# Kernel optimization log

Measured on AMD Instinct MI355X. Metric: run time of the kernel, lower is better.

The kernel has to match this reference:

```python
import jax, jax.numpy as jnp
import numpy as np

N_NODES = 50000
N_EDGES = 200000
D_IN = 128
D = 256
N_LAYERS = 4
N_REL = 4
NUM_M = 1024
NUM_R = 64
DIM_Y = 2
LAM_VI = 0.1
LAM_REG = 0.1
TEMP = 0.3  # RelaxedBernoulli temperature used by FNP sample_bipartite
EPS = 1e-8


def _glorot(key, shape):
    fan_in = shape[-2] if len(shape) >= 2 else shape[0]
    return (jax.random.normal(key, shape, dtype=jnp.float32) / np.float32(np.sqrt(fan_in)))


def setup_inputs() -> dict:
    key = jax.random.key(0)
    ks = jax.random.split(key, 16)
    x = jax.random.normal(ks[0], (N_NODES, D_IN), jnp.float32)
    edge_index = jax.random.randint(ks[1], (2, N_EDGES), 0, N_NODES)
    edge_type = jax.random.randint(ks[2], (N_EDGES,), 0, N_REL)
    batch = jnp.sort(jax.random.randint(ks[3], (N_NODES,), 0, NUM_M))
    yM = jax.random.randint(ks[4], (NUM_M,), 0, DIM_Y)
    yR = jax.random.randint(ks[5], (NUM_R,), 0, DIM_Y)
    H_R = jax.random.normal(ks[6], (NUM_R, D), jnp.float32)
    node_W = _glorot(ks[7], (D_IN, D)); node_b = jnp.zeros((D,), jnp.float32)
    gcn_Wr = _glorot(ks[8], (N_LAYERS, N_REL, D, D))
    gcn_Wroot = _glorot(ks[9], (N_LAYERS, D, D))
    gcn_b = jnp.zeros((N_LAYERS, D), jnp.float32)
    pg_logscale = jnp.array([0.5 * np.log(D)], jnp.float32)  # log(sqrt(dim_u)) init
    pu_W = _glorot(ks[10], (D, 2 * D)); pu_b = jnp.zeros((2 * D,), jnp.float32)
    qz_W = _glorot(ks[11], (D, 2 * D)); qz_b = jnp.zeros((2 * D,), jnp.float32)
    out_W1 = _glorot(ks[12], (2 * D, 256)); out_b1 = jnp.zeros((256,), jnp.float32)
    out_W2 = _glorot(ks[13], (256, DIM_Y)); out_b2 = jnp.zeros((DIM_Y,), jnp.float32)
    return dict(x=x, edge_index=edge_index, edge_type=edge_type, batch=batch, yM=yM, yR=yR,
                H_R=H_R, node_W=node_W, node_b=node_b, gcn_Wr=gcn_Wr, gcn_Wroot=gcn_Wroot,
                gcn_b=gcn_b, pg_logscale=pg_logscale, pu_W=pu_W, pu_b=pu_b, qz_W=qz_W,
                qz_b=qz_b, out_W1=out_W1, out_b1=out_b1, out_W2=out_W2, out_b2=out_b2)


def _cond_trans(x, edge_index, edge_type, batch, node_W, node_b, gcn_Wr, gcn_Wroot, gcn_b):
    # AtomEncoder replaced by Linear (num_relations==1 branch); then 4 RGCNConv layers
    n = x.shape[0]
    src, dst = edge_index[0], edge_index[1]
    feats = x @ node_W + node_b
    for l in range(N_LAYERS):
        # per-relation transform of all nodes: [N_REL, N, D]
        h_rel = jnp.einsum('nd,rdh->rnh', feats, gcn_Wr[l])
        msg = h_rel[edge_type, src]  # gather per-edge messages [E, D]
        comp = edge_type * n + dst   # (relation, dst) composite segment id
        cnt = jax.ops.segment_sum(jnp.ones((msg.shape[0],), feats.dtype), comp,
                                  num_segments=N_REL * n)
        msg = msg / jnp.clip(cnt[comp], 1.0)[:, None]  # mean aggregation per relation
        agg = jax.ops.segment_sum(msg, dst, num_segments=n)
        feats = agg + feats @ gcn_Wroot[l] + gcn_b[l]
        if l < N_LAYERS - 1:
            feats = jax.nn.relu(feats)
    gsum = jax.ops.segment_sum(feats, batch, num_segments=NUM_M)
    gcnt = jax.ops.segment_sum(jnp.ones((n,), feats.dtype), batch, num_segments=NUM_M)
    return gsum / jnp.clip(gcnt, 1.0)[:, None]  # global_mean_pool


def _normal_logprob(v, mean, logscale):
    return -0.5 * np.float32(np.log(2 * np.pi)) - logscale - 0.5 * ((v - mean) * jnp.exp(-logscale)) ** 2


def _logitexp(logp):
    # logit of exp(logp): logp - log(1 - exp(logp))
    return logp - jnp.log(jnp.clip(-jnp.expm1(logp), 1e-20))


def reference(x, edge_index, edge_type, batch, yM, yR, H_R, node_W, node_b, gcn_Wr,
              gcn_Wroot, gcn_b, pg_logscale, pu_W, pu_b, qz_W, qz_b, out_W1, out_b1,
              out_W2, out_b2):
    H_M = _cond_trans(x, edge_index, edge_type, batch, node_W, node_b, gcn_Wr, gcn_Wroot, gcn_b)
    H_all = jnp.concatenate([H_R, H_M], axis=0)
    key = jax.random.key(42)
    k_u, k_a, k_zm, k_zr = jax.random.split(key, 4)

    # p_u: ReLU -> Linear -> split mean / logscale; reparameterized sample
    pu = jax.nn.relu(H_all) @ pu_W + pu_b
    pu_mean, pu_ls = pu[:, :D], pu[:, D:]
    u = pu_mean + jnp.exp(pu_ls) * jax.random.normal(k_u, pu_mean.shape, pu_mean.dtype)
    u_R, u_M = u[:NUM_R], u[NUM_R:]

    # sample_bipartite(u_M, u_R, pairwise_g): relaxed Bernoulli over pairwise logits
    d2 = jnp.sum((u_M[:, None, :] - u_R[None, :, :]) ** 2, axis=-1)  # [M, R]
    logits_A = _logitexp(-0.5 * d2 / jnp.exp(pg_logscale[0]))
    U = jax.random.uniform(k_a, logits_A.shape, minval=1e-6, maxval=1.0 - 1e-6)
    A = jax.nn.sigmoid((logits_A + jnp.log(U) - jnp.log1p(-U)) / TEMP)
    An = A / (jnp.sum(A, axis=1, keepdims=True) + EPS)  # norm_graph

    # q_z head
    qz = jax.nn.relu(H_all) @ qz_W + qz_b
    qz_mean, qz_ls = qz[:, :D], qz[:, D:]
    z_M = qz_mean[NUM_R:] + jnp.exp(qz_ls[NUM_R:]) * jax.random.normal(k_zm, (NUM_M, D), qz_mean.dtype)
    pz_mean_M = An @ qz_mean[:NUM_R]
    pz_ls_M = An @ qz_ls[:NUM_R]
    log_pqz_M = jnp.sum(_normal_logprob(z_M, pz_mean_M, pz_ls_M)
                        - _normal_logprob(z_M, qz_mean[NUM_R:], qz_ls[NUM_R:]))
    z_R = qz_mean[:NUM_R] + jnp.exp(qz_ls[:NUM_R]) * jax.random.normal(k_zr, (NUM_R, D), qz_mean.dtype)

    # prediction head (use_plus=True -> concat z and u)
    rep_M = jnp.concatenate([z_M, u_M], axis=1)
    logits_M = jax.nn.relu(rep_M @ out_W1 + out_b1) @ out_W2 + out_b2
    log_pyM = jnp.take_along_axis(jax.nn.log_softmax(logits_M, axis=-1), yM[:, None], axis=1)[:, 0]
    prediction_loss = -(jnp.sum(log_pyM) + LAM_VI * log_pqz_M) / np.float32(NUM_M)

    rep_R = jnp.concatenate([z_R, u_R], axis=1)
    logits_R = jax.nn.relu(rep_R @ out_W1 + out_b1) @ out_W2 + out_b2
    rationale_loss = -jnp.mean(jnp.take_along_axis(jax.nn.log_softmax(logits_R, axis=-1), yR[:, None], axis=1)[:, 0])

    # mode 'E' distance regularizer
    pd = jnp.sqrt(jnp.clip(jnp.sum((u_R[:, None, :] - u_M[None, :, :]) ** 2, axis=-1), 1e-12))  # [R, M]
    idx = jnp.arange(NUM_R // 2)[:, None] + (1 - yM)[None, :] * (NUM_R // 2)
    reg = jnp.mean(jnp.take_along_axis(pd, idx, axis=0))

    return prediction_loss + rationale_loss - LAM_REG * reg
```

## Files before the change

### kernel.cpp

```cpp
#include <hip/hip_runtime.h>
#include <stdint.h>

#define N_NODESC 50000
#define N_EDGESC 200000
#define D_INC 128
#define DC 256
#define N_LAYERSC 4
#define N_RELC 4
#define NUM_MC 1024
#define NUM_RC 64
#define NBLK_SCAN ((N_NODESC + 255) / 256)

typedef __attribute__((ext_vector_type(4))) float floatx4;
typedef __attribute__((ext_vector_type(8))) short short8;

__host__ __device__ __forceinline__ uint32_t rotl32(uint32_t x, int r){ return (x<<r)|(x>>(32-r)); }

__host__ __device__ inline void tf2x32(uint32_t k0, uint32_t k1, uint32_t x0, uint32_t x1,
                                       uint32_t* o0, uint32_t* o1){
  uint32_t k2 = k0 ^ k1 ^ 0x1BD11BDAu;
#define TFR(r) { x0 += x1; x1 = rotl32(x1, (r)); x1 ^= x0; }
  x0 += k0; x1 += k1;
  TFR(13) TFR(15) TFR(26) TFR(6)
  x0 += k1; x1 += k2 + 1u;
  TFR(17) TFR(29) TFR(16) TFR(24)
  x0 += k2; x1 += k0 + 2u;
  TFR(13) TFR(15) TFR(26) TFR(6)
  x0 += k0; x1 += k1 + 3u;
  TFR(17) TFR(29) TFR(16) TFR(24)
  x0 += k1; x1 += k2 + 4u;
  TFR(13) TFR(15) TFR(26) TFR(6)
  x0 += k2; x1 += k0 + 5u;
#undef TFR
  *o0 = x0; *o1 = x1;
}

__device__ __forceinline__ float erfinv_f32(float x){
  float w = -log1pf(-x*x);
  float p;
  if (w < 5.0f){
    w -= 2.5f;
    p = 2.81022636e-08f;
    p = fmaf(p, w, 3.43273939e-07f);
    p = fmaf(p, w, -3.5233877e-06f);
    p = fmaf(p, w, -4.39150654e-06f);
    p = fmaf(p, w, 0.00021858087f);
    p = fmaf(p, w, -0.00125372503f);
    p = fmaf(p, w, -0.00417768164f);
    p = fmaf(p, w, 0.246640727f);
    p = fmaf(p, w, 1.50140941f);
  } else {
    w = sqrtf(w) - 3.0f;
    p = -0.000200214257f;
    p = fmaf(p, w, 0.000100950558f);
    p = fmaf(p, w, 0.00134934322f);
    p = fmaf(p, w, -0.00367342844f);
    p = fmaf(p, w, 0.00573950773f);
    p = fmaf(p, w, -0.0076224613f);
    p = fmaf(p, w, 0.00943887047f);
    p = fmaf(p, w, 1.00167406f);
    p = fmaf(p, w, 2.83297682f);
  }
  return p*x;
}

__device__ __forceinline__ float bits_to_unit(uint32_t b){
  return __uint_as_float((b >> 9) | 0x3f800000u) - 1.0f;
}

__device__ __forceinline__ float bits_to_normal(uint32_t b){
  float f = bits_to_unit(b);
  const float lo = -0.99999994f;
  float u = f * (1.0f - lo) + lo;
  u = fmaxf(u, lo);
  return 1.41421356f * erfinv_f32(u);
}

__device__ __forceinline__ float waveReduce(float v){
  #pragma unroll
  for (int m = 1; m < 64; m <<= 1) v += __shfl_xor(v, m, 64);
  return v;
}

__device__ __forceinline__ ushort f2bf(float f){
  uint32_t u = __float_as_uint(f);
  uint32_t r = u + 0x7fffu + ((u>>16)&1u);
  return (ushort)(r>>16);
}
__device__ __forceinline__ float bf2f(ushort h){
  return __uint_as_float(((uint32_t)h)<<16);
}

typedef const __attribute__((address_space(1))) void* gas_t;
typedef __attribute__((address_space(3))) void* las_t;
__device__ __forceinline__ void gld16(const void* g, void* l){
  __builtin_amdgcn_global_load_lds((gas_t)g, (las_t)l, 16, 0, 0);
}

__global__ __launch_bounds__(256) void k_zero4(float4* p, int n4){
  int i = blockIdx.x*256 + threadIdx.x;
  if (i < n4) p[i] = make_float4(0.f,0.f,0.f,0.f);
}

__global__ __launch_bounds__(256) void k_count(const int* __restrict__ ei, const int* __restrict__ et,
                                               float* __restrict__ cnt, int* __restrict__ deg){
  int e = blockIdx.x*256 + threadIdx.x;
  if (e >= N_EDGESC) return;
  int r = et[e], dstv = ei[N_EDGESC + e];
  atomicAdd(&cnt[(size_t)r*N_NODESC + dstv], 1.0f);
  atomicAdd(&deg[dstv], 1);
}

__global__ __launch_bounds__(256) void k_scan1(const int* __restrict__ deg, int* __restrict__ bsum){
  int i = blockIdx.x*256 + threadIdx.x;
  int v = (i < N_NODESC) ? deg[i] : 0;
  #pragma unroll
  for (int m = 1; m < 64; m <<= 1) v += __shfl_xor(v, m, 64);
  __shared__ int ws_[4];
  if ((threadIdx.x & 63) == 0) ws_[threadIdx.x >> 6] = v;
  __syncthreads();
  if (threadIdx.x == 0) bsum[blockIdx.x] = ws_[0]+ws_[1]+ws_[2]+ws_[3];
}

__global__ __launch_bounds__(256) void k_scan2(int* __restrict__ bsum, int* __restrict__ boff){
  __shared__ int s[256];
  int t = threadIdx.x;
  s[t] = (t < NBLK_SCAN) ? bsum[t] : 0;
  __syncthreads();
  if (t == 0){
    int run = 0;
    for (int i = 0; i < NBLK_SCAN; i++){ int v = s[i]; s[i] = run; run += v; }
  }
  __syncthreads();
  if (t < NBLK_SCAN) boff[t] = s[t];
}

__global__ __launch_bounds__(256) void k_scan3(const int* __restrict__ deg, const int* __restrict__ boff,
                                               int* __restrict__ rowptr){
  int i = blockIdx.x*256 + threadIdx.x;
  int lane = threadIdx.x & 63, w = threadIdx.x >> 6;
  int d = (i < N_NODESC) ? deg[i] : 0;
  int v = d;
  #pragma unroll
  for (int off = 1; off < 64; off <<= 1){
    int t = __shfl_up(v, off, 64);
    if (lane >= off) v += t;
  }
  __shared__ int wt[4];
  if (lane == 63) wt[w] = v;
  __syncthreads();
  int wo = 0;
  for (int k = 0; k < w; k++) wo += wt[k];
  int ex = boff[blockIdx.x] + wo + v - d;
  if (i <= N_NODESC) rowptr[i] = ex;
}

__global__ __launch_bounds__(256) void k_fill2(const int* __restrict__ ei, const int* __restrict__ et,
                                               const float* __restrict__ cnt, const int* __restrict__ rowptr,
                                               int* __restrict__ cursor, int* __restrict__ ep,
                                               float* __restrict__ einvc){
  int e = blockIdx.x*256 + threadIdx.x;
  if (e >= N_EDGESC) return;
  int src = ei[e], dstv = ei[N_EDGESC + e], r = et[e];
  int pos = rowptr[dstv] + atomicAdd(&cursor[dstv], 1);
  ep[pos] = src | (r << 16);
  einvc[pos] = 1.0f / fmaxf(cnt[(size_t)r*N_NODESC + dstv], 1.0f);
}

__global__ __launch_bounds__(256) void k_bnd(const int* __restrict__ batch, int* __restrict__ grow){
  int i = blockIdx.x*256 + threadIdx.x;
  if (i >= N_NODESC) return;
  int b = batch[i];
  if (i == 0){ for (int g = 0; g <= b; g++) grow[g] = 0; }
  else {
    int pb = batch[i-1];
    for (int g = pb+1; g <= b; g++) grow[g] = i;
  }
  if (i == N_NODESC-1){ for (int g = b+1; g <= NUM_MC; g++) grow[g] = N_NODESC; }
}

#define SEG0 (N_NODESC*D_INC/4)
#define SEG1 (DC*D_INC)
#define SEG2 (N_LAYERSC*DC*1280)
#define SEG3 (DC*1024)
#define SEG4 (DC*512)
#define SEG5 1024
__global__ __launch_bounds__(256) void k_prep(const float* __restrict__ x, ushort* __restrict__ xb,
                                              const float* __restrict__ node_W, ushort* __restrict__ node_Wt,
                                              const float* __restrict__ Wroot, const float* __restrict__ Wr,
                                              ushort* __restrict__ Wcat,
                                              const float* __restrict__ pu_W, const float* __restrict__ qz_W,
                                              float* __restrict__ pqW,
                                              const float* __restrict__ out_W1, ushort* __restrict__ W1t,
                                              const float* __restrict__ pu_b, const float* __restrict__ qz_b,
                                              float* __restrict__ pqb){
  int idx = blockIdx.x*256 + threadIdx.x;
  if (idx < SEG0){
    float4 v = ((const float4*)x)[idx];
    ushort4 o; o.x=f2bf(v.x); o.y=f2bf(v.y); o.z=f2bf(v.z); o.w=f2bf(v.w);
    ((ushort4*)xb)[idx] = o;
    return;
  }
  idx -= SEG0;
  if (idx < SEG1){
    int n = idx >> 7, k = idx & 127;
    node_Wt[idx] = f2bf(node_W[(size_t)k*DC + n]);
    return;
  }
  idx -= SEG1;
  if (idx < SEG2){
    int l = idx / (DC*1280), rem = idx - l*(DC*1280);
    int n = rem / 1280, k = rem - n*1280;
    float v;
    if (k < DC) v = Wroot[((size_t)l*DC + k)*DC + n];
    else {
      int kk = k - DC, r = kk >> 8, kr = kk & 255;
      v = Wr[(((size_t)l*N_RELC + r)*DC + kr)*DC + n];
    }
    Wcat[idx] = f2bf(v);
    return;
  }
  idx -= SEG2;
  if (idx < SEG3){
    int k = idx >> 10, n = idx & 1023;
    pqW[idx] = (n < 512) ? pu_W[(size_t)k*512 + n] : qz_W[(size_t)k*512 + (n-512)];
    return;
  }
  idx -= SEG3;
  if (idx < SEG4){
    int n = idx >> 9, k = idx & 511;
    W1t[idx] = f2bf(out_W1[(size_t)k*DC + n]);
    return;
  }
  idx -= SEG4;
  if (idx < SEG5){
    pqb[idx] = (idx < 512) ? pu_b[idx] : qz_b[idx-512];
  }
}

__global__ __launch_bounds__(256) void k_agg(const ushort* __restrict__ curb, ushort* __restrict__ agg,
                                             const int* __restrict__ rowptr, const int* __restrict__ ep,
                                             const float* __restrict__ einvc){
  int dstv = blockIdx.x*4 + (threadIdx.x >> 6);
  if (dstv >= N_NODESC) return;
  int lane = threadIdx.x & 63;
  int beg = rowptr[dstv], end = rowptr[dstv+1];
  float4 s0 = {0,0,0,0}, s1 = {0,0,0,0}, s2 = {0,0,0,0}, s3 = {0,0,0,0};
  int p = beg;
  while (p < end){
    int nb = end - p; if (nb > 8) nb = 8;
    int pk[8]; float ic[8]; ushort4 h[8];
    #pragma unroll
    for (int j = 0; j < 8; j++) if (j < nb){ pk[j] = ep[p+j]; ic[j] = einvc[p+j]; }
    #pragma unroll
    for (int j = 0; j < 8; j++) if (j < nb)
      h[j] = *(const ushort4*)(curb + (size_t)(pk[j] & 0xffff)*DC + lane*4);
    #pragma unroll
    for (int j = 0; j < 8; j++) if (j < nb){
      float c = ic[j];
      int r = pk[j] >> 16;
      float hx = bf2f(h[j].x)*c, hy = bf2f(h[j].y)*c, hz = bf2f(h[j].z)*c, hw = bf2f(h[j].w)*c;
      if (r == 0){ s0.x+=hx; s0.y+=hy; s0.z+=hz; s0.w+=hw; }
      else if (r == 1){ s1.x+=hx; s1.y+=hy; s1.z+=hz; s1.w+=hw; }
      else if (r == 2){ s2.x+=hx; s2.y+=hy; s2.z+=hz; s2.w+=hw; }
      else { s3.x+=hx; s3.y+=hy; s3.z+=hz; s3.w+=hw; }
    }
    p += nb;
  }
  ushort* ab = agg + (size_t)dstv*1024 + lane*4;
  ushort4 o;
  o.x=f2bf(s0.x); o.y=f2bf(s0.y); o.z=f2bf(s0.z); o.w=f2bf(s0.w); *(ushort4*)(ab       ) = o;
  o.x=f2bf(s1.x); o.y=f2bf(s1.y); o.z=f2bf(s1.z); o.w=f2bf(s1.w); *(ushort4*)(ab + 256 ) = o;
  o.x=f2bf(s2.x); o.y=f2bf(s2.y); o.z=f2bf(s2.z); o.w=f2bf(s2.w); *(ushort4*)(ab + 512 ) = o;
  o.x=f2bf(s3.x); o.y=f2bf(s3.y); o.z=f2bf(s3.z); o.w=f2bf(s3.w); *(ushort4*)(ab + 768 ) = o;
}

__global__ __launch_bounds__(256) void k_pool(const ushort* __restrict__ featsb, const int* __restrict__ grow,
                                              const float* __restrict__ H_R, float* __restrict__ Hrelu){
  int row = blockIdx.x*4 + (threadIdx.x >> 6);
  if (row >= NUM_RC + NUM_MC) return;
  int lane = threadIdx.x & 63;
  float4 v;
  if (row < NUM_RC){
    v = *(const float4*)(H_R + (size_t)row*DC + lane*4);
  } else {
    int g = row - NUM_RC;
    int beg = grow[g], end = grow[g+1];
    float ax=0.f, ay=0.f, az=0.f, aw=0.f;
    for (int i = beg; i < end; i++){
      const ushort4 f = *(const ushort4*)(featsb + (size_t)i*DC + lane*4);
      ax += bf2f(f.x); ay += bf2f(f.y); az += bf2f(f.z); aw += bf2f(f.w);
    }
    float ic = 1.0f / fmaxf((float)(end-beg), 1.0f);
    v.x = ax*ic; v.y = ay*ic; v.z = az*ic; v.w = aw*ic;
  }
  v.x = fmaxf(v.x,0.f); v.y = fmaxf(v.y,0.f); v.z = fmaxf(v.z,0.f); v.w = fmaxf(v.w,0.f);
  *(float4*)(Hrelu + (size_t)row*DC + lane*4) = v;
}

__global__ __launch_bounds__(256) void k_gemm_bf16(
    const ushort* __restrict__ A1, int lda1,
    const ushort* __restrict__ A2, int lda2, int Ksplit,
    const ushort* __restrict__ Bt, int ldb,
    void* __restrict__ Cout0, int ldc,
    int M, int N, int K,
    const float* __restrict__ bias, int flags)
{
  __shared__ ushort As[64*64];
  __shared__ ushort Bs[128*64];
  const int tid = threadIdx.x;
  const int wave = tid >> 6, lane = tid & 63;
  const int m0 = blockIdx.y * 64, n0 = blockIdx.x * 128;
  const int wn = wave * 32;
  const int qa = lane >> 4, lm = lane & 15;

  const int lrow = lane >> 3;
  const int slot = lane & 7;

  floatx4 acc[4][2] = {};

  for (int k0 = 0; k0 < K; k0 += 64){
    const ushort* a_base; int a_ld, acol;
    if (k0 < Ksplit){ a_base = A1; a_ld = lda1; acol = k0; }
    else            { a_base = A2; a_ld = lda2; acol = k0 - Ksplit; }
    #pragma unroll
    for (int t = 0; t < 2; t++){
      int rb = wave*16 + t*8;
      int rr = rb + lrow;
      int gl = slot ^ (rr & 7);
      int ar = m0 + rr; if (ar > M-1) ar = M-1;
      gld16(a_base + (size_t)ar*a_ld + acol + gl*8, As + (size_t)rb*64 + lane*8);
    }
    #pragma unroll
    for (int t = 0; t < 4; t++){
      int rb = wave*32 + t*8;
      int rr = rb + lrow;
      int gl = slot ^ (rr & 7);
      gld16(Bt + (size_t)(n0 + rr)*ldb + k0 + gl*8, Bs + (size_t)rb*64 + lane*8);
    }
    __syncthreads();
    #pragma unroll
    for (int kk2 = 0; kk2 < 2; kk2++){
      short8 af[4], bfv[2];
      #pragma unroll
      for (int mt = 0; mt < 4; mt++){
        int rr = mt*16 + lm;
        af[mt] = *(const short8*)(As + (size_t)rr*64 + (size_t)(((kk2*4 + qa) ^ (rr & 7)))*8);
      }
      #pragma unroll
      for (int nt = 0; nt < 2; nt++){
        int rr = wn + nt*16 + lm;
        bfv[nt] = *(const short8*)(Bs + (size_t)rr*64 + (size_t)(((kk2*4 + qa) ^ (rr & 7)))*8);
      }
      #pragma unroll
      for (int mt = 0; mt < 4; mt++)
        #pragma unroll
        for (int nt = 0; nt < 2; nt++)
          acc[mt][nt] = __builtin_amdgcn_mfma_f32_16x16x32_bf16(af[mt], bfv[nt], acc[mt][nt], 0, 0, 0);
    }
    __syncthreads();
  }

  #pragma unroll
  for (int mt = 0; mt < 4; mt++){
    #pragma unroll
    for (int i = 0; i < 4; i++){
      int row = m0 + mt*16 + qa*4 + i;
      if (row >= M) continue;
      #pragma unroll
      for (int nt = 0; nt < 2; nt++){
        int col = n0 + wn + nt*16 + lm;
        float v = acc[mt][nt][i];
        if (flags & 2) v += bias[col];
        if (flags & 4) v = fmaxf(v, 0.0f);
        if (flags & 1)
          ((ushort*)Cout0)[(size_t)row*ldc + col] = f2bf(v);
        else
          ((float*)Cout0)[(size_t)row*ldc + col] = v;
      }
    }
  }
}

__global__ __launch_bounds__(256) void k_gemm(
    const float* __restrict__ A, int lda,
    const float* __restrict__ B, int ldb,
    float* __restrict__ C, int ldc,
    int M, int N, int K,
    const float* __restrict__ bias, int flags)
{
  __shared__ __align__(16) float Asm[64][36];
  __shared__ __align__(16) float Bsm[32][64];
  const int tid = threadIdx.x;
  const int tx = tid & 15, ty = tid >> 4;
  const int m0 = blockIdx.y * 64, n0 = blockIdx.x * 64;
  const int am = tid >> 2, ak = (tid & 3) * 8;
  const int bk = tid >> 3, bn = (tid & 7) * 8;
  float acc[4][4] = {};
  for (int k0 = 0; k0 < K; k0 += 32){
    float4 a0, a1;
    int arow = m0 + am;
    if (arow < M){
      const float* ap = A + (size_t)arow*lda + (k0 + ak);
      a0 = *(const float4*)ap;
      a1 = *(const float4*)(ap + 4);
    } else {
      a0 = make_float4(0,0,0,0); a1 = a0;
    }
    const float* bp = B + (size_t)(k0 + bk)*ldb + (n0 + bn);
    float4 b0v = *(const float4*)bp;
    float4 b1v = *(const float4*)(bp + 4);
    *(float4*)&Asm[am][ak]   = a0;
    *(float4*)&Asm[am][ak+4] = a1;
    *(float4*)&Bsm[bk][bn]   = b0v;
    *(float4*)&Bsm[bk][bn+4] = b1v;
    __syncthreads();
    #pragma unroll
    for (int kk = 0; kk < 32; ++kk){
      float av[4], bv[4];
      #pragma unroll
      for (int i=0;i<4;i++) av[i] = Asm[ty*4+i][kk];
      #pragma unroll
      for (int j=0;j<4;j++) bv[j] = Bsm[kk][tx*4+j];
      #pragma unroll
      for (int i=0;i<4;i++)
        #pragma unroll
        for (int j=0;j<4;j++)
          acc[i][j] = fmaf(av[i], bv[j], acc[i][j]);
    }
    __syncthreads();
  }
  #pragma unroll
  for (int i=0;i<4;i++){
    int row = m0 + ty*4 + i;
    if (row >= M) continue;
    #pragma unroll
    for (int j=0;j<4;j++){
      int col = n0 + tx*4 + j;
      float v = acc[i][j];
      if (flags & 2) v += bias[col];
      if (flags & 4) v = fmaxf(v, 0.0f);
      C[(size_t)row*ldc + col] = v;
    }
  }
}

__global__ __launch_bounds__(256) void k_sample_u(const float* __restrict__ pq, float* __restrict__ u,
                                                  ushort* __restrict__ repb,
                                                  uint32_t k0, uint32_t k1){
  const int half = (1088*DC)/2;
  int j = blockIdx.x*256 + threadIdx.x;
  if (j >= half) return;
  uint32_t o0, o1;
  tf2x32(k0, k1, (uint32_t)j, (uint32_t)(j + half), &o0, &o1);
  #pragma unroll
  for (int t = 0; t < 2; t++){
    int i = j + t*half;
    uint32_t bits = t ? o1 : o0;
    int row = i >> 8, col = i & 255;
    const float* pr = pq + (size_t)row*1024;
    float val = pr[col] + expf(pr[256 + col]) * bits_to_normal(bits);
    u[i] = val;
    repb[(size_t)row*512 + 256 + col] = f2bf(val);
  }
}

__global__ __launch_bounds__(256) void k_sample_zM(const float* __restrict__ pq, float* __restrict__ zM,
                                                   ushort* __restrict__ repb,
                                                   uint32_t k0, uint32_t k1){
  const int half = (NUM_MC*DC)/2;
  int j = blockIdx.x*256 + threadIdx.x;
  if (j >= half) return;
  uint32_t o0, o1;
  tf2x32(k0, k1, (uint32_t)j, (uint32_t)(j + half), &o0, &o1);
  #pragma unroll
  for (int t = 0; t < 2; t++){
    int i = j + t*half;
    uint32_t bits = t ? o1 : o0;
    int m = i >> 8, col = i & 255;
    const float* pr = pq + (size_t)(NUM_RC + m)*1024;
    float val = pr[512 + col] + expf(pr[768 + col]) * bits_to_normal(bits);
    zM[i] = val;
    repb[(size_t)(NUM_RC + m)*512 + col] = f2bf(val);
  }
}

__global__ __launch_bounds__(256) void k_sample_zR(const float* __restrict__ pq, ushort* __restrict__ repb,
                                                   uint32_t k0, uint32_t k1){
  const int half = (NUM_RC*DC)/2;
  int j = blockIdx.x*256 + threadIdx.x;
  if (j >= half) return;
  uint32_t o0, o1;
  tf2x32(k0, k1, (uint32_t)j, (uint32_t)(j + half), &o0, &o1);
  #pragma unroll
  for (int t = 0; t < 2; t++){
    int i = j + t*half;
    uint32_t bits = t ? o1 : o0;
    int r = i >> 8, col = i & 255;
    const float* pr = pq + (size_t)r*1024;
    float val = pr[512 + col] + expf(pr[768 + col]) * bits_to_normal(bits);
    repb[(size_t)r*512 + col] = f2bf(val);
  }
}

__global__ __launch_bounds__(64) void k_d2(const float* __restrict__ u, float* __restrict__ d2){
  int m = blockIdx.x, r = threadIdx.x;
  const float4* um = (const float4*)(u + (size_t)(NUM_RC + m)*DC);
  const float4* ur = (const float4*)(u + (size_t)r*DC);
  float s = 0.f;
  #pragma unroll 4
  for (int d = 0; d < DC/4; ++d){
    float4 a = um[d], b = ur[d];
    float dx = a.x-b.x, dy = a.y-b.y, dz = a.z-b.z, dw = a.w-b.w;
    s = fmaf(dx,dx, fmaf(dy,dy, fmaf(dz,dz, fmaf(dw,dw, s))));
  }
  d2[m*NUM_RC + r] = s;
}

__device__ __forceinline__ void A_elem(float* An, const float* d2, int i, uint32_t bits, float inv_s){
  float logp = -0.5f * d2[i] * inv_s;
  float la = logp - logf(fmaxf(-expm1f(logp), 1e-20f));
  float f = bits_to_unit(bits);
  const float mn = 1e-6f, mx = 0.999999f;
  float U = fmaxf(f*(mx-mn) + mn, mn);
  float g = (la + logf(U) - log1pf(-U)) / 0.3f;
  An[i] = 1.0f / (1.0f + expf(-g));
}

__global__ __launch_bounds__(256) void k_A(const float* __restrict__ d2, const float* __restrict__ pg,
                                           float* __restrict__ An, uint32_t k0, uint32_t k1){
  const int HALF = (NUM_MC*NUM_RC)/2;
  int j = blockIdx.x*256 + threadIdx.x;
  if (j >= HALF) return;
  uint32_t o0, o1;
  tf2x32(k0, k1, (uint32_t)j, (uint32_t)(j + HALF), &o0, &o1);
  float inv_s = expf(-pg[0]);
  A_elem(An, d2, j, o0, inv_s);
  A_elem(An, d2, j + HALF, o1, inv_s);
}

__global__ __launch_bounds__(64) void k_rownorm(float* __restrict__ An){
  int m = blockIdx.x, r = threadIdx.x;
  float v = An[m*NUM_RC + r];
  float s = waveReduce(v);
  An[m*NUM_RC + r] = v / (s + 1e-8f);
}

__global__ __launch_bounds__(256) void k_logpqz(const float* __restrict__ zM, const float* __restrict__ pzcat,
                                                const float* __restrict__ pq, float* __restrict__ scal){
  int idx = blockIdx.x*256 + threadIdx.x;
  int m = idx >> 8, d = idx & 255;
  float z  = zM[idx];
  float pm = pzcat[(size_t)m*512 + d];
  float pl = pzcat[(size_t)m*512 + 256 + d];
  const float* qrow = pq + (size_t)(NUM_RC + m)*1024;
  float qm = qrow[512 + d], ql = qrow[768 + d];
  float tp = (z - pm) * expf(-pl);
  float tq = (z - qm) * expf(-ql);
  float term = (-pl - 0.5f*tp*tp) - (-ql - 0.5f*tq*tq);
  float s = waveReduce(term);
  if ((threadIdx.x & 63) == 0) atomicAdd(&scal[0], s);
}

__global__ __launch_bounds__(256) void k_out_head(const float* __restrict__ hid, const float* __restrict__ W2,
                                                  const float* __restrict__ b2, const int* __restrict__ yM,
                                                  const int* __restrict__ yR, float* __restrict__ scal){
  int wave = threadIdx.x >> 6, lane = threadIdx.x & 63;
  int row = blockIdx.x*4 + wave;
  if (row >= NUM_RC + NUM_MC) return;
  const float* h = hid + (size_t)row*256;
  float p0 = 0.f, p1 = 0.f;
  #pragma unroll
  for (int c = 0; c < 4; c++){
    int d = lane*4 + c;
    float hv = h[d];
    p0 = fmaf(hv, W2[d*2+0], p0);
    p1 = fmaf(hv, W2[d*2+1], p1);
  }
  p0 = waveReduce(p0);
  p1 = waveReduce(p1);
  if (lane == 0){
    float l0 = p0 + b2[0], l1 = p1 + b2[1];
    float mx = fmaxf(l0, l1);
    float lse = mx + logf(expf(l0-mx) + expf(l1-mx));
    int y = (row < NUM_RC) ? yR[row] : yM[row - NUM_RC];
    float lp = ((y == 0) ? l0 : l1) - lse;
    atomicAdd((row < NUM_RC) ? &scal[2] : &scal[1], lp);
  }
}

__global__ __launch_bounds__(256) void k_reg(const float* __restrict__ d2, const int* __restrict__ yM,
                                             float* __restrict__ scal){
  int t = blockIdx.x*256 + threadIdx.x;
  float v = 0.f;
  if (t < 32*1024){
    int i = t >> 10, m = t & 1023;
    int col = i + (1 - yM[m]) * 32;
    v = sqrtf(fmaxf(d2[m*NUM_RC + col], 1e-12f));
  }
  float s = waveReduce(v);
  if ((threadIdx.x & 63) == 0) atomicAdd(&scal[3], s);
}

__global__ void k_final(const float* __restrict__ scal, float* __restrict__ out){
  float pred = -(scal[1] + 0.1f*scal[0]) / 1024.0f;
  float rat  = -scal[2] / 64.0f;
  float regm = scal[3] / 32768.0f;
  out[0] = pred + rat - 0.1f*regm;
}

extern "C" void kernel_launch(void* const* d_in, const int* in_sizes, int n_in,
                              void* d_out, int out_size, void* d_ws, size_t ws_size,
                              hipStream_t stream) {
  const float* x         = (const float*)d_in[0];
  const int*   edge_index= (const int*)  d_in[1];
  const int*   edge_type = (const int*)  d_in[2];
  const int*   batch     = (const int*)  d_in[3];
  const int*   yM        = (const int*)  d_in[4];
  const int*   yR        = (const int*)  d_in[5];
  const float* H_R       = (const float*)d_in[6];
  const float* node_W    = (const float*)d_in[7];
  const float* node_b    = (const float*)d_in[8];
  const float* gcn_Wr    = (const float*)d_in[9];
  const float* gcn_Wroot = (const float*)d_in[10];
  const float* gcn_b     = (const float*)d_in[11];
  const float* pg_ls     = (const float*)d_in[12];
  const float* pu_W      = (const float*)d_in[13];
  const float* pu_b      = (const float*)d_in[14];
  const float* qz_W      = (const float*)d_in[15];
  const float* qz_b      = (const float*)d_in[16];
  const float* out_W1    = (const float*)d_in[17];
  const float* out_b1    = (const float*)d_in[18];
  const float* out_W2    = (const float*)d_in[19];
  const float* out_b2    = (const float*)d_in[20];
  float* out = (float*)d_out;

  char* base = (char*)d_ws;
  size_t off = 0;
  auto ALLOC = [&](size_t nbytes)->void*{
    void* p = base + off; off += (nbytes + 255) & ~(size_t)255; return p;
  };
  ushort* curb_a  = (ushort*)ALLOC((size_t)N_NODESC*DC*2);
  ushort* curb_b  = (ushort*)ALLOC((size_t)N_NODESC*DC*2);
  ushort* agg     = (ushort*)ALLOC((size_t)N_NODESC*1024*2);
  ushort* xb      = (ushort*)ALLOC((size_t)N_NODESC*D_INC*2);
  ushort* node_Wt = (ushort*)ALLOC((size_t)SEG1*2);
  ushort* Wcat    = (ushort*)ALLOC((size_t)SEG2*2);
  float*  pqW     = (float*) ALLOC((size_t)SEG3*4);
  ushort* W1t     = (ushort*)ALLOC((size_t)SEG4*2);
  float*  pqb     = (float*) ALLOC((size_t)SEG5*4);
  float*  zgrp    = (float*) ALLOC((size_t)(N_RELC*N_NODESC + N_NODESC + N_NODESC + 16)*4);
  float*  cnt     = zgrp;
  int*    deg     = (int*)(cnt + (size_t)N_RELC*N_NODESC);
  int*    cursor  = deg + N_NODESC;
  float*  scal    = (float*)(cursor + N_NODESC);
  int*    rowptr  = (int*)   ALLOC((size_t)(N_NODESC+1)*4);
  int*    bsum    = (int*)   ALLOC((size_t)NBLK_SCAN*4);
  int*    boff    = (int*)   ALLOC((size_t)NBLK_SCAN*4);
  int*    ep      = (int*)   ALLOC((size_t)N_EDGESC*4);
  float*  einvc   = (float*) ALLOC((size_t)N_EDGESC*4);
  int*    grow    = (int*)   ALLOC((size_t)(NUM_MC+1)*4);
  float*  Hrelu   = (float*) ALLOC((size_t)1088*DC*4);
  float*  pq      = (float*) ALLOC((size_t)1088*1024*4);
  float*  u       = (float*) ALLOC((size_t)1088*DC*4);
  ushort* repb    = (ushort*)ALLOC((size_t)1088*512*2);
  float*  zM      = (float*) ALLOC((size_t)NUM_MC*DC*4);
  float*  d2      = (float*) ALLOC((size_t)NUM_MC*NUM_RC*4);
  float*  An      = (float*) ALLOC((size_t)NUM_MC*NUM_RC*4);
  float*  pzcat   = (float*) ALLOC((size_t)NUM_MC*512*4);
  float*  hid     = (float*) ALLOC((size_t)1088*256*4);
  (void)ws_size; (void)in_sizes; (void)n_in; (void)out_size;

  uint32_t ya0,ya1,yb0,yb1,yc0,yc1,yd0,yd1;
  tf2x32(0u,42u, 0u,4u, &ya0,&ya1);
  tf2x32(0u,42u, 1u,5u, &yb0,&yb1);
  tf2x32(0u,42u, 2u,6u, &yc0,&yc1);
  tf2x32(0u,42u, 3u,7u, &yd0,&yd1);
  const uint32_t ku0=ya0,  ku1=yb0;
  const uint32_t ka0=yc0,  ka1=yd0;
  const uint32_t kzm0=ya1, kzm1=yb1;
  const uint32_t kzr0=yc1, kzr1=yd1;

  auto GEMM = [&](const float* A, int lda, const float* B, int ldb, float* C, int ldc,
                  int M, int N, int K, const float* bias, int flags){
    k_gemm<<<dim3(N/64, (M+63)/64), dim3(256), 0, stream>>>(A, lda, B, ldb, C, ldc, M, N, K, bias, flags);
  };
  auto BGEMM = [&](const ushort* A1, int lda1, const ushort* A2, int lda2, int Ksplit,
                   const ushort* Bt, int ldb, void* C, int ldc,
                   int M, int N, int K, const float* bias, int flags){
    k_gemm_bf16<<<dim3(N/128, (M+63)/64), dim3(256), 0, stream>>>(
        A1, lda1, A2, lda2, Ksplit, Bt, ldb, C, ldc, M, N, K, bias, flags);
  };

  {
    int n4 = (N_RELC*N_NODESC + 2*N_NODESC + 16)/4;
    k_zero4<<<dim3((n4+255)/256), dim3(256), 0, stream>>>((float4*)zgrp, n4);
  }
  k_count<<<dim3((N_EDGESC+255)/256), dim3(256), 0, stream>>>(edge_index, edge_type, cnt, deg);
  k_scan1<<<dim3(NBLK_SCAN), dim3(256), 0, stream>>>(deg, bsum);
  k_scan2<<<dim3(1), dim3(256), 0, stream>>>(bsum, boff);
  k_scan3<<<dim3(NBLK_SCAN), dim3(256), 0, stream>>>(deg, boff, rowptr);
  k_fill2<<<dim3((N_EDGESC+255)/256), dim3(256), 0, stream>>>(edge_index, edge_type, cnt, rowptr, cursor, ep, einvc);
  k_bnd  <<<dim3((N_NODESC+255)/256), dim3(256), 0, stream>>>(batch, grow);
  {
    int total = SEG0+SEG1+SEG2+SEG3+SEG4+SEG5;
    k_prep<<<dim3((total+255)/256), dim3(256), 0, stream>>>(
        x, xb, node_W, node_Wt, gcn_Wroot, gcn_Wr, Wcat, pu_W, qz_W, pqW, out_W1, W1t, pu_b, qz_b, pqb);
  }

  BGEMM(xb, D_INC, xb, D_INC, D_INC, node_Wt, D_INC, curb_a, DC, N_NODESC, DC, D_INC, node_b, 1|2);

  ushort* cur = curb_a; ushort* nxt = curb_b;
  for (int l = 0; l < N_LAYERSC; l++){
    k_agg<<<dim3((N_NODESC+3)/4), dim3(256), 0, stream>>>(cur, agg, rowptr, ep, einvc);
    int fl = 1 | 2 | ((l < N_LAYERSC-1) ? 4 : 0);
    BGEMM(cur, DC, agg, 1024, DC, Wcat + (size_t)l*DC*1280, 1280, nxt, DC,
          N_NODESC, DC, 1280, gcn_b + l*DC, fl);
    ushort* t = nxt; nxt = cur; cur = t;
  }

  k_pool<<<dim3((NUM_RC+NUM_MC+3)/4), dim3(256), 0, stream>>>(cur, grow, H_R, Hrelu);

  GEMM(Hrelu, DC, pqW, 1024, pq, 1024, 1088, 1024, DC, pqb, 2);

  k_sample_u<<<dim3(544), dim3(256), 0, stream>>>(pq, u, repb, ku0, ku1);

  k_d2<<<dim3(NUM_MC), dim3(64), 0, stream>>>(u, d2);
  k_A <<<dim3(128), dim3(256), 0, stream>>>(d2, pg_ls, An, ka0, ka1);
  k_rownorm<<<dim3(NUM_MC), dim3(64), 0, stream>>>(An);

  GEMM(An, NUM_RC, pq + 512, 1024, pzcat, 512, NUM_MC, 512, NUM_RC, nullptr, 0);

  k_sample_zM<<<dim3(512), dim3(256), 0, stream>>>(pq, zM, repb, kzm0, kzm1);
  k_logpqz<<<dim3(1024), dim3(256), 0, stream>>>(zM, pzcat, pq, scal);
  k_sample_zR<<<dim3(32), dim3(256), 0, stream>>>(pq, repb, kzr0, kzr1);

  BGEMM(repb, 512, repb, 512, 512, W1t, 512, hid, 256, NUM_RC+NUM_MC, 256, 512, out_b1, 2|4);
  k_out_head<<<dim3((NUM_RC+NUM_MC)/4), dim3(256), 0, stream>>>(hid, out_W2, out_b2, yM, yR, scal);

  k_reg<<<dim3(128), dim3(256), 0, stream>>>(d2, yM, scal);
  k_final<<<dim3(1), dim3(1), 0, stream>>>(scal, out);
}
```

Measured before the change: 742.0 us.

## Use half-wave-per-node aggregation, 8-wave bf16 GEMM, and batched pool loads

The aggregation kernel now gives each destination node 32 lanes that load 8 bf16 values each, so 8 nodes run per block with wider 16-byte gathers and FMA accumulation. The bf16 GEMM moves from 4 to 8 waves per block on the same 64x128 tile, which halves the per-wave accumulator footprint and the per-thread tile loads. The pooling loop batches 4 row loads at a time to expose more memory parallelism. These changes aim at the memory-bound gather and the GEMM's latency hiding, at the cost of more register-heavy aggregation lanes and more waves sharing the same LDS tile.

```diff
diff --git a/kernel.cpp b/kernel.cpp
--- a/kernel.cpp
+++ b/kernel.cpp
@@ -241,38 +241,55 @@
 __global__ __launch_bounds__(256) void k_agg(const ushort* __restrict__ curb, ushort* __restrict__ agg,
                                              const int* __restrict__ rowptr, const int* __restrict__ ep,
                                              const float* __restrict__ einvc){
-  int dstv = blockIdx.x*4 + (threadIdx.x >> 6);
+  int halfid = threadIdx.x >> 5;
+  int dstv = blockIdx.x*8 + halfid;
   if (dstv >= N_NODESC) return;
-  int lane = threadIdx.x & 63;
+  int lane = threadIdx.x & 31;
   int beg = rowptr[dstv], end = rowptr[dstv+1];
-  float4 s0 = {0,0,0,0}, s1 = {0,0,0,0}, s2 = {0,0,0,0}, s3 = {0,0,0,0};
+  float s0[8] = {}, s1[8] = {}, s2[8] = {}, s3[8] = {};
   int p = beg;
   while (p < end){
     int nb = end - p; if (nb > 8) nb = 8;
-    int pk[8]; float ic[8]; ushort4 h[8];
+    int pk[8]; float ic[8]; short8 h[8];
     #pragma unroll
     for (int j = 0; j < 8; j++) if (j < nb){ pk[j] = ep[p+j]; ic[j] = einvc[p+j]; }
     #pragma unroll
     for (int j = 0; j < 8; j++) if (j < nb)
-      h[j] = *(const ushort4*)(curb + (size_t)(pk[j] & 0xffff)*DC + lane*4);
+      h[j] = *(const short8*)(curb + (size_t)(pk[j] & 0xffff)*DC + lane*8);
     #pragma unroll
     for (int j = 0; j < 8; j++) if (j < nb){
       float c = ic[j];
       int r = pk[j] >> 16;
-      float hx = bf2f(h[j].x)*c, hy = bf2f(h[j].y)*c, hz = bf2f(h[j].z)*c, hw = bf2f(h[j].w)*c;
-      if (r == 0){ s0.x+=hx; s0.y+=hy; s0.z+=hz; s0.w+=hw; }
-      else if (r == 1){ s1.x+=hx; s1.y+=hy; s1.z+=hz; s1.w+=hw; }
-      else if (r == 2){ s2.x+=hx; s2.y+=hy; s2.z+=hz; s2.w+=hw; }
-      else { s3.x+=hx; s3.y+=hy; s3.z+=hz; s3.w+=hw; }
+      if (r == 0){
+        #pragma unroll
+        for (int e = 0; e < 8; e++) s0[e] = fmaf(bf2f((ushort)h[j][e]), c, s0[e]);
+      } else if (r == 1){
+        #pragma unroll
+        for (int e = 0; e < 8; e++) s1[e] = fmaf(bf2f((ushort)h[j][e]), c, s1[e]);
+      } else if (r == 2){
+        #pragma unroll
+        for (int e = 0; e < 8; e++) s2[e] = fmaf(bf2f((ushort)h[j][e]), c, s2[e]);
+      } else {
+        #pragma unroll
+        for (int e = 0; e < 8; e++) s3[e] = fmaf(bf2f((ushort)h[j][e]), c, s3[e]);
+      }
     }
     p += nb;
   }
-  ushort* ab = agg + (size_t)dstv*1024 + lane*4;
-  ushort4 o;
-  o.x=f2bf(s0.x); o.y=f2bf(s0.y); o.z=f2bf(s0.z); o.w=f2bf(s0.w); *(ushort4*)(ab       ) = o;
-  o.x=f2bf(s1.x); o.y=f2bf(s1.y); o.z=f2bf(s1.z); o.w=f2bf(s1.w); *(ushort4*)(ab + 256 ) = o;
-  o.x=f2bf(s2.x); o.y=f2bf(s2.y); o.z=f2bf(s2.z); o.w=f2bf(s2.w); *(ushort4*)(ab + 512 ) = o;
-  o.x=f2bf(s3.x); o.y=f2bf(s3.y); o.z=f2bf(s3.z); o.w=f2bf(s3.w); *(ushort4*)(ab + 768 ) = o;
+  ushort* ab = agg + (size_t)dstv*1024 + lane*8;
+  short8 o;
+  #pragma unroll
+  for (int e = 0; e < 8; e++) o[e] = (short)f2bf(s0[e]);
+  *(short8*)(ab      ) = o;
+  #pragma unroll
+  for (int e = 0; e < 8; e++) o[e] = (short)f2bf(s1[e]);
+  *(short8*)(ab + 256) = o;
+  #pragma unroll
+  for (int e = 0; e < 8; e++) o[e] = (short)f2bf(s2[e]);
+  *(short8*)(ab + 512) = o;
+  #pragma unroll
+  for (int e = 0; e < 8; e++) o[e] = (short)f2bf(s3[e]);
+  *(short8*)(ab + 768) = o;
 }
 
 __global__ __launch_bounds__(256) void k_pool(const ushort* __restrict__ featsb, const int* __restrict__ grow,
@@ -287,9 +304,18 @@
     int g = row - NUM_RC;
     int beg = grow[g], end = grow[g+1];
     float ax=0.f, ay=0.f, az=0.f, aw=0.f;
-    for (int i = beg; i < end; i++){
-      const ushort4 f = *(const ushort4*)(featsb + (size_t)i*DC + lane*4);
-      ax += bf2f(f.x); ay += bf2f(f.y); az += bf2f(f.z); aw += bf2f(f.w);
+    int i = beg;
+    while (i < end){
+      int nb = end - i; if (nb > 4) nb = 4;
+      ushort4 f[4];
+      #pragma unroll
+      for (int j = 0; j < 4; j++) if (j < nb)
+        f[j] = *(const ushort4*)(featsb + (size_t)(i+j)*DC + lane*4);
+      #pragma unroll
+      for (int j = 0; j < 4; j++) if (j < nb){
+        ax += bf2f(f[j].x); ay += bf2f(f[j].y); az += bf2f(f[j].z); aw += bf2f(f[j].w);
+      }
+      i += nb;
     }
     float ic = 1.0f / fmaxf((float)(end-beg), 1.0f);
     v.x = ax*ic; v.y = ay*ic; v.z = az*ic; v.w = aw*ic;
@@ -298,7 +324,7 @@
   *(float4*)(Hrelu + (size_t)row*DC + lane*4) = v;
 }
 
-__global__ __launch_bounds__(256) void k_gemm_bf16(
+__global__ __launch_bounds__(512) void k_gemm_bf16(
     const ushort* __restrict__ A1, int lda1,
     const ushort* __restrict__ A2, int lda2, int Ksplit,
     const ushort* __restrict__ Bt, int ldb,
@@ -311,40 +337,39 @@
   const int tid = threadIdx.x;
   const int wave = tid >> 6, lane = tid & 63;
   const int m0 = blockIdx.y * 64, n0 = blockIdx.x * 128;
-  const int wn = wave * 32;
+  const int wm = (wave >> 2) * 32;
+  const int wn = (wave & 3) * 32;
   const int qa = lane >> 4, lm = lane & 15;
 
   const int lrow = lane >> 3;
   const int slot = lane & 7;
 
-  floatx4 acc[4][2] = {};
+  floatx4 acc[2][2] = {};
 
   for (int k0 = 0; k0 < K; k0 += 64){
     const ushort* a_base; int a_ld, acol;
     if (k0 < Ksplit){ a_base = A1; a_ld = lda1; acol = k0; }
     else            { a_base = A2; a_ld = lda2; acol = k0 - Ksplit; }
+    {
+      int rr = wave*8 + lrow;
+      int gl = slot ^ (rr & 7);
+      int ar = m0 + rr; if (ar > M-1) ar = M-1;
+      gld16(a_base + (size_t)ar*a_ld + acol + gl*8, As + (size_t)(wave*8)*64 + lane*8);
+    }
     #pragma unroll
     for (int t = 0; t < 2; t++){
       int rb = wave*16 + t*8;
       int rr = rb + lrow;
       int gl = slot ^ (rr & 7);
-      int ar = m0 + rr; if (ar > M-1) ar = M-1;
-      gld16(a_base + (size_t)ar*a_ld + acol + gl*8, As + (size_t)rb*64 + lane*8);
-    }
-    #pragma unroll
-    for (int t = 0; t < 4; t++){
-      int rb = wave*32 + t*8;
-      int rr = rb + lrow;
-      int gl = slot ^ (rr & 7);
       gld16(Bt + (size_t)(n0 + rr)*ldb + k0 + gl*8, Bs + (size_t)rb*64 + lane*8);
     }
     __syncthreads();
     #pragma unroll
     for (int kk2 = 0; kk2 < 2; kk2++){
-      short8 af[4], bfv[2];
-      #pragma unroll
-      for (int mt = 0; mt < 4; mt++){
-        int rr = mt*16 + lm;
+      short8 af[2], bfv[2];
+      #pragma unroll
+      for (int mt = 0; mt < 2; mt++){
+        int rr = wm + mt*16 + lm;
         af[mt] = *(const short8*)(As + (size_t)rr*64 + (size_t)(((kk2*4 + qa) ^ (rr & 7)))*8);
       }
       #pragma unroll
@@ -353,7 +378,7 @@
         bfv[nt] = *(const short8*)(Bs + (size_t)rr*64 + (size_t)(((kk2*4 + qa) ^ (rr & 7)))*8);
       }
       #pragma unroll
-      for (int mt = 0; mt < 4; mt++)
+      for (int mt = 0; mt < 2; mt++)
         #pragma unroll
         for (int nt = 0; nt < 2; nt++)
           acc[mt][nt] = __builtin_amdgcn_mfma_f32_16x16x32_bf16(af[mt], bfv[nt], acc[mt][nt], 0, 0, 0);
@@ -362,10 +387,10 @@
   }
 
   #pragma unroll
-  for (int mt = 0; mt < 4; mt++){
+  for (int mt = 0; mt < 2; mt++){
     #pragma unroll
     for (int i = 0; i < 4; i++){
-      int row = m0 + mt*16 + qa*4 + i;
+      int row = m0 + wm + mt*16 + qa*4 + i;
       if (row >= M) continue;
       #pragma unroll
       for (int nt = 0; nt < 2; nt++){
@@ -688,7 +713,7 @@
   auto BGEMM = [&](const ushort* A1, int lda1, const ushort* A2, int lda2, int Ksplit,
                    const ushort* Bt, int ldb, void* C, int ldc,
                    int M, int N, int K, const float* bias, int flags){
-    k_gemm_bf16<<<dim3(N/128, (M+63)/64), dim3(256), 0, stream>>>(
+    k_gemm_bf16<<<dim3(N/128, (M+63)/64), dim3(512), 0, stream>>>(
         A1, lda1, A2, lda2, Ksplit, Bt, ldb, C, ldc, M, N, K, bias, flags);
   };
 
@@ -712,7 +737,7 @@
 
   ushort* cur = curb_a; ushort* nxt = curb_b;
   for (int l = 0; l < N_LAYERSC; l++){
-    k_agg<<<dim3((N_NODESC+3)/4), dim3(256), 0, stream>>>(cur, agg, rowptr, ep, einvc);
+    k_agg<<<dim3((N_NODESC+7)/8), dim3(256), 0, stream>>>(cur, agg, rowptr, ep, einvc);
     int fl = 1 | 2 | ((l < N_LAYERSC-1) ? 4 : 0);
     BGEMM(cur, DC, agg, 1024, DC, Wcat + (size_t)l*DC*1280, 1280, nxt, DC,
           N_NODESC, DC, 1280, gcn_b + l*DC, fl);
```

Result: faster. 707.4 us, median of 2 (-4.7%).
